# Kernel optimization log

Hardware: AMD Instinct MI355X
Metric: run time of the kernel (lower is better)

Reference implementation:

```python
import jax, jax.numpy as jnp
import numpy as np

IN_FEATURES = 4096
OUT_FEATURES = 11008
TOKENS = 32


def ternarize_weight(w):
    # abs-mean scale, clamped; threshold at 0.7*abs_mean
    abs_mean = jnp.maximum(jnp.mean(jnp.abs(w)), 1e-5)
    threshold = 0.7 * abs_mean
    q = jnp.where(w > threshold, 1.0, jnp.where(w < -threshold, -1.0, 0.0))
    # straight-through estimator: forward value q*abs_mean, grad passes to w
    return w + jax.lax.stop_gradient(q * abs_mean - w)


def setup_inputs() -> dict:
    key = jax.random.key(0)
    kx, kw = jax.random.split(key)
    x = jax.random.normal(kx, (TOKENS, IN_FEATURES), dtype=jnp.float32)
    # master fp32 weights, init std = 1/sqrt(in_features) as in the module
    weight = jax.random.normal(kw, (OUT_FEATURES, IN_FEATURES), dtype=jnp.float32) / np.sqrt(IN_FEATURES)
    return {"x": x, "weight": weight}


def reference(x, weight):
    # ternary_active=True, ternary_alpha=1.0 path: fully ternarized weights
    w_q = ternarize_weight(weight)
    # F.linear(x, w): [T, in] @ [out, in]^T -> [T, out]
    return jnp.einsum('ti,oi->to', x, w_q)
```

## Files before the change

### kernel.cpp

```cpp
#include <hip/hip_runtime.h>
#include <hip/hip_bf16.h>
#include <stdint.h>

#define IN_F 4096
#define OUT_F 11008
#define TOKENS 32
#define NELEM_W (OUT_F * IN_F)

typedef __attribute__((ext_vector_type(8))) __bf16 bf16x8;
typedef __attribute__((ext_vector_type(4))) float  f32x4;

__global__ __launch_bounds__(256) void absum_kernel(const float* __restrict__ w,
                                                    double* __restrict__ ws_sum) {
    int tid = blockIdx.x * blockDim.x + threadIdx.x;
    int stride = gridDim.x * blockDim.x;
    const float4* w4 = (const float4*)w;
    const int n4 = NELEM_W / 4;
    float s = 0.f;
    for (int i = tid; i < n4; i += stride) {
        float4 v = w4[i];
        s += fabsf(v.x) + fabsf(v.y) + fabsf(v.z) + fabsf(v.w);
    }
    for (int off = 32; off > 0; off >>= 1)
        s += __shfl_down(s, off, 64);
    __shared__ float wsum[4];
    int lane = threadIdx.x & 63;
    int wv   = threadIdx.x >> 6;
    if (lane == 0) wsum[wv] = s;
    __syncthreads();
    if (threadIdx.x == 0) {
        float t = wsum[0] + wsum[1] + wsum[2] + wsum[3];
        atomicAdd(ws_sum, (double)t);
    }
}

__global__ void finalize_kernel(double* __restrict__ ws) {
    double mean = ws[0] / (double)NELEM_W;
    if (mean < 1e-5) mean = 1e-5;
    float mf = (float)mean;
    float* f = (float*)ws;
    f[2] = 0.7f * mf;
    f[3] = mf;
}

__device__ __forceinline__ uint32_t tern1(float v, float thr) {
    uint32_t u  = __float_as_uint(v);
    uint32_t pm = (u & 0x80000000u) | 0x3F800000u;
    return (__builtin_fabsf(v) > thr) ? pm : 0u;
}

__device__ __forceinline__ bf16x8 tern8(float4 b0, float4 b1, float thr) {
    uint32_t q0 = tern1(b0.x, thr), q1 = tern1(b0.y, thr);
    uint32_t q2 = tern1(b0.z, thr), q3 = tern1(b0.w, thr);
    uint32_t q4 = tern1(b1.x, thr), q5 = tern1(b1.y, thr);
    uint32_t q6 = tern1(b1.z, thr), q7 = tern1(b1.w, thr);
    union { uint32_t u[4]; bf16x8 v; } U;
    U.u[0] = (q0 >> 16) | (q1 & 0xFFFF0000u);
    U.u[1] = (q2 >> 16) | (q3 & 0xFFFF0000u);
    U.u[2] = (q4 >> 16) | (q5 & 0xFFFF0000u);
    U.u[3] = (q6 >> 16) | (q7 & 0xFFFF0000u);
    return U.v;
}

__device__ __forceinline__ uint32_t bfr(float v) {
    uint32_t u = __float_as_uint(v);
    uint32_t r = u + 0x7FFFu + ((u >> 16) & 1u);
    return r >> 16;
}

__device__ __forceinline__ bf16x8 cvt8(float4 a0, float4 a1) {
    union { uint32_t u[4]; bf16x8 v; } U;
    U.u[0] = bfr(a0.x) | (bfr(a0.y) << 16);
    U.u[1] = bfr(a0.z) | (bfr(a0.w) << 16);
    U.u[2] = bfr(a1.x) | (bfr(a1.y) << 16);
    U.u[3] = bfr(a1.z) | (bfr(a1.w) << 16);
    return U.v;
}

#define KSPLIT 8
#define KCHUNK (IN_F / KSPLIT)
#define KSTEPS (KCHUNK / 32)

__global__ __launch_bounds__(64, 4) void ternary_gemm(const float* __restrict__ x,
                                                      const float* __restrict__ w,
                                                      const float* __restrict__ wsf,
                                                      float* __restrict__ out) {
    const float thr   = wsf[2];
    const float scale = wsf[3];
    const int bid  = blockIdx.x;
    const int og   = bid >> 3;
    const int kc   = bid & (KSPLIT - 1);
    const int lane = threadIdx.x;
    const int col  = lane & 15;
    const int quad = lane >> 4;

    const float* wp  = w + (size_t)(og * 16 + col) * IN_F + kc * KCHUNK + quad * 8;
    const float* xp0 = x + (size_t)col * IN_F + kc * KCHUNK + quad * 8;
    const float* xp1 = xp0 + (size_t)16 * IN_F;

    f32x4 acc0 = {0.f, 0.f, 0.f, 0.f};
    f32x4 acc1 = {0.f, 0.f, 0.f, 0.f};

#pragma unroll 4
    for (int s = 0; s < KSTEPS; ++s) {
        float4 b0 = *(const float4*)(wp);
        float4 b1 = *(const float4*)(wp + 4);
        float4 a0 = *(const float4*)(xp0);
        float4 a1 = *(const float4*)(xp0 + 4);
        float4 a2 = *(const float4*)(xp1);
        float4 a3 = *(const float4*)(xp1 + 4);
        wp  += 32;
        xp0 += 32;
        xp1 += 32;

        bf16x8 bf  = tern8(b0, b1, thr);
        bf16x8 af0 = cvt8(a0, a1);
        bf16x8 af1 = cvt8(a2, a3);

        acc0 = __builtin_amdgcn_mfma_f32_16x16x32_bf16(af0, bf, acc0, 0, 0, 0);
        acc1 = __builtin_amdgcn_mfma_f32_16x16x32_bf16(af1, bf, acc1, 0, 0, 0);
    }

    const int obase = og * 16 + col;
#pragma unroll
    for (int r = 0; r < 4; ++r) {
        int t0 = quad * 4 + r;
        atomicAdd(out + (size_t)t0 * OUT_F + obase,        scale * acc0[r]);
        atomicAdd(out + (size_t)(t0 + 16) * OUT_F + obase, scale * acc1[r]);
    }
}

extern "C" void kernel_launch(void* const* d_in, const int* in_sizes, int n_in,
                              void* d_out, int out_size, void* d_ws, size_t ws_size,
                              hipStream_t stream) {
    const float* x = (const float*)d_in[0];
    const float* w = (const float*)d_in[1];
    float* out     = (float*)d_out;
    double* wsd    = (double*)d_ws;

    hipMemsetAsync(d_ws, 0, 16, stream);
    hipMemsetAsync(d_out, 0, sizeof(float) * TOKENS * OUT_F, stream);

    absum_kernel<<<2048, 256, 0, stream>>>(w, wsd);
    finalize_kernel<<<1, 1, 0, stream>>>(wsd);
    ternary_gemm<<<(OUT_F / 16) * KSPLIT, 64, 0, stream>>>(x, w, (const float*)d_ws, out);
}
```

Baseline: 336.4 us.

## Pre-convert x to bf16 and reduce K-split in-block instead of atomics

```diff
diff --git a/kernel.cpp b/kernel.cpp
--- a/kernel.cpp
+++ b/kernel.cpp
@@ -10,10 +10,34 @@
 typedef __attribute__((ext_vector_type(8))) __bf16 bf16x8;
 typedef __attribute__((ext_vector_type(4))) float  f32x4;
 
-__global__ __launch_bounds__(256) void absum_kernel(const float* __restrict__ w,
-                                                    double* __restrict__ ws_sum) {
+__device__ __forceinline__ uint32_t bfr(float v) {
+    uint32_t u = __float_as_uint(v);
+    uint32_t r = u + 0x7FFFu + ((u >> 16) & 1u);
+    return r >> 16;
+}
+
+#define ABSUM_BLOCKS 2048
+#define XCVT_BLOCKS  64
+
+__global__ __launch_bounds__(256) void absum_xcvt_kernel(const float* __restrict__ w,
+                                                         const float* __restrict__ x,
+                                                         double* __restrict__ ws_sum,
+                                                         uint4* __restrict__ xb) {
+    if (blockIdx.x >= ABSUM_BLOCKS) {
+        int i = (blockIdx.x - ABSUM_BLOCKS) * 256 + threadIdx.x;
+        const float4* x4 = (const float4*)x;
+        float4 a0 = x4[i * 2];
+        float4 a1 = x4[i * 2 + 1];
+        uint4 o;
+        o.x = bfr(a0.x) | (bfr(a0.y) << 16);
+        o.y = bfr(a0.z) | (bfr(a0.w) << 16);
+        o.z = bfr(a1.x) | (bfr(a1.y) << 16);
+        o.w = bfr(a1.z) | (bfr(a1.w) << 16);
+        xb[i] = o;
+        return;
+    }
     int tid = blockIdx.x * blockDim.x + threadIdx.x;
-    int stride = gridDim.x * blockDim.x;
+    int stride = ABSUM_BLOCKS * 256;
     const float4* w4 = (const float4*)w;
     const int n4 = NELEM_W / 4;
     float s = 0.f;
@@ -62,41 +86,26 @@
     return U.v;
 }
 
-__device__ __forceinline__ uint32_t bfr(float v) {
-    uint32_t u = __float_as_uint(v);
-    uint32_t r = u + 0x7FFFu + ((u >> 16) & 1u);
-    return r >> 16;
-}
+#define KSTEPS 32
 
-__device__ __forceinline__ bf16x8 cvt8(float4 a0, float4 a1) {
-    union { uint32_t u[4]; bf16x8 v; } U;
-    U.u[0] = bfr(a0.x) | (bfr(a0.y) << 16);
-    U.u[1] = bfr(a0.z) | (bfr(a0.w) << 16);
-    U.u[2] = bfr(a1.x) | (bfr(a1.y) << 16);
-    U.u[3] = bfr(a1.z) | (bfr(a1.w) << 16);
-    return U.v;
-}
-
-#define KSPLIT 8
-#define KCHUNK (IN_F / KSPLIT)
-#define KSTEPS (KCHUNK / 32)
-
-__global__ __launch_bounds__(64, 4) void ternary_gemm(const float* __restrict__ x,
-                                                      const float* __restrict__ w,
-                                                      const float* __restrict__ wsf,
-                                                      float* __restrict__ out) {
+__global__ __launch_bounds__(256) void ternary_gemm(const float* __restrict__ w,
+                                                    const float* __restrict__ wsf,
+                                                    const __bf16* __restrict__ xb,
+                                                    float* __restrict__ out) {
+    __shared__ float red[4 * 512];
     const float thr   = wsf[2];
     const float scale = wsf[3];
-    const int bid  = blockIdx.x;
-    const int og   = bid >> 3;
-    const int kc   = bid & (KSPLIT - 1);
-    const int lane = threadIdx.x;
+    const int og   = blockIdx.x;
+    const int tid  = threadIdx.x;
+    const int wv   = tid >> 6;
+    const int lane = tid & 63;
     const int col  = lane & 15;
     const int quad = lane >> 4;
 
-    const float* wp  = w + (size_t)(og * 16 + col) * IN_F + kc * KCHUNK + quad * 8;
-    const float* xp0 = x + (size_t)col * IN_F + kc * KCHUNK + quad * 8;
-    const float* xp1 = xp0 + (size_t)16 * IN_F;
+    const int kbase = wv * 1024 + quad * 8;
+    const float*  wp  = w  + (size_t)(og * 16 + col) * IN_F + kbase;
+    const __bf16* xp0 = xb + (size_t)col * IN_F + kbase;
+    const __bf16* xp1 = xp0 + (size_t)16 * IN_F;
 
     f32x4 acc0 = {0.f, 0.f, 0.f, 0.f};
     f32x4 acc1 = {0.f, 0.f, 0.f, 0.f};
@@ -105,28 +114,35 @@
     for (int s = 0; s < KSTEPS; ++s) {
         float4 b0 = *(const float4*)(wp);
         float4 b1 = *(const float4*)(wp + 4);
-        float4 a0 = *(const float4*)(xp0);
-        float4 a1 = *(const float4*)(xp0 + 4);
-        float4 a2 = *(const float4*)(xp1);
-        float4 a3 = *(const float4*)(xp1 + 4);
+        bf16x8 a0 = *(const bf16x8*)(xp0);
+        bf16x8 a1 = *(const bf16x8*)(xp1);
         wp  += 32;
         xp0 += 32;
         xp1 += 32;
 
-        bf16x8 bf  = tern8(b0, b1, thr);
-        bf16x8 af0 = cvt8(a0, a1);
-        bf16x8 af1 = cvt8(a2, a3);
-
-        acc0 = __builtin_amdgcn_mfma_f32_16x16x32_bf16(af0, bf, acc0, 0, 0, 0);
-        acc1 = __builtin_amdgcn_mfma_f32_16x16x32_bf16(af1, bf, acc1, 0, 0, 0);
+        bf16x8 bf = tern8(b0, b1, thr);
+        acc0 = __builtin_amdgcn_mfma_f32_16x16x32_bf16(a0, bf, acc0, 0, 0, 0);
+        acc1 = __builtin_amdgcn_mfma_f32_16x16x32_bf16(a1, bf, acc1, 0, 0, 0);
     }
 
-    const int obase = og * 16 + col;
+    {
+        float* base = red + wv * 512;
 #pragma unroll
-    for (int r = 0; r < 4; ++r) {
-        int t0 = quad * 4 + r;
-        atomicAdd(out + (size_t)t0 * OUT_F + obase,        scale * acc0[r]);
-        atomicAdd(out + (size_t)(t0 + 16) * OUT_F + obase, scale * acc1[r]);
+        for (int r = 0; r < 4; ++r) base[r * 64 + lane]       = acc0[r];
+#pragma unroll
+        for (int r = 0; r < 4; ++r) base[256 + r * 64 + lane] = acc1[r];
+    }
+    __syncthreads();
+
+#pragma unroll
+    for (int p = tid; p < 512; p += 256) {
+        int t = p >> 4, c = p & 15;
+        int a = t >> 4;
+        int q = (t >> 2) & 3;
+        int r = t & 3;
+        int idx = a * 256 + r * 64 + q * 16 + c;
+        float s = red[idx] + red[512 + idx] + red[1024 + idx] + red[1536 + idx];
+        out[(size_t)t * OUT_F + og * 16 + c] = s * scale;
     }
 }
 
@@ -137,11 +153,12 @@
     const float* w = (const float*)d_in[1];
     float* out     = (float*)d_out;
     double* wsd    = (double*)d_ws;
+    uint4* xb      = (uint4*)((char*)d_ws + 64);
 
     hipMemsetAsync(d_ws, 0, 16, stream);
-    hipMemsetAsync(d_out, 0, sizeof(float) * TOKENS * OUT_F, stream);
 
-    absum_kernel<<<2048, 256, 0, stream>>>(w, wsd);
+    absum_xcvt_kernel<<<ABSUM_BLOCKS + XCVT_BLOCKS, 256, 0, stream>>>(w, x, wsd, xb);
     finalize_kernel<<<1, 1, 0, stream>>>(wsd);
-    ternary_gemm<<<(OUT_F / 16) * KSPLIT, 64, 0, stream>>>(x, w, (const float*)d_ws, out);
+    ternary_gemm<<<OUT_F / 16, 256, 0, stream>>>(w, (const float*)d_ws,
+                                                 (const __bf16*)((char*)d_ws + 64), out);
 }
```

Result: faster. 305.9 us (-9.1%).
